# Kernel tuning notes

Hardware: AMD Instinct MI355X
Metric: run time of the kernel (lower is better)

Reference implementation:

```python
import jax, jax.numpy as jnp
import numpy as np

K = 2.0          # arctan surrogate sharpness (init kwarg k)
THRESHOLD = 1.0  # init kwarg threshold


def _binop(ei, ej):
    # linear recurrence combine: (A, Bu) pairs, v_t = A_t*v_{t-1} + Bu_t
    a_i, b_i = ei
    a_j, b_j = ej
    return a_j * a_i, a_j * b_i + b_j


def _pscan(tau, x):
    # x: [B, T, H]; tau: [H] broadcast over batch and time (matches
    # jnp.repeat(tau[None], T, 0) inside vmap over batch in the original).
    tau_b = jnp.broadcast_to(tau, x.shape)
    _, v = jax.lax.associative_scan(_binop, (tau_b, x), axis=1)
    return v


@jax.custom_vjp
def _spike(x):
    # spyx arctan surrogate: forward is Heaviside, backward 1/(1+(k*x)^2)
    return jnp.where(x > 0, 1.0, 0.0).astype(x.dtype)


def _spike_fwd(x):
    return _spike(x), x


def _spike_bwd(x, g):
    return (g / (1.0 + (K * x) ** 2),)


_spike.defvjp(_spike_fwd, _spike_bwd)


def setup_inputs() -> dict:
    key = jax.random.key(0)
    k1, k2 = jax.random.split(key)
    x = jax.random.normal(k1, (16, 1024, 1024), dtype=jnp.float32)
    # beta ~ TruncatedNormal(mean=0.25, std=0.5), as in hk.initializers
    beta = 0.25 + 0.5 * jax.random.truncated_normal(k2, -2.0, 2.0, (1024,), jnp.float32)
    return {"x": x, "beta": beta}


def reference(x, beta):
    b = jnp.clip(beta, 0.0, 1.0)
    V = _pscan(b, x)                      # membrane potential scan
    R = _pscan(b, jax.nn.sigmoid(V))      # refractory/reset scan
    return _spike(V - R - THRESHOLD), V
```

## Files before the change

kernel.cpp:

```cpp
#include <hip/hip_runtime.h>


#define BB 16
#define TT 1024
#define HH 1024
#define UNR 32

__global__ __launch_bounds__(64) void lif_scan(const float* __restrict__ x,
                                               const float* __restrict__ beta,
                                               float* __restrict__ out_spike,
                                               float* __restrict__ out_v) {
    const int tid = blockIdx.x * blockDim.x + threadIdx.x;
    const int b = tid >> 10;
    const int h = tid & (HH - 1);

    const float bf = fminf(fmaxf(beta[h], 0.0f), 1.0f);
    const double bd = (double)bf;

    const size_t base = (size_t)b * TT * HH + (size_t)h;
    const float* __restrict__ xp = x + base;
    float* __restrict__ sp = out_spike + base;
    float* __restrict__ vp = out_v + base;

    double V = 0.0, R = 0.0;

    float xbuf[UNR];
#pragma unroll
    for (int i = 0; i < UNR; ++i) xbuf[i] = xp[(size_t)i * HH];

#pragma unroll 1
    for (int t0 = 0; t0 < TT; t0 += UNR) {
        float xnext[UNR];
        const bool more = (t0 + UNR) < TT;
        if (more) {
#pragma unroll
            for (int i = 0; i < UNR; ++i)
                xnext[i] = xp[(size_t)(t0 + UNR + i) * HH];
        }
#pragma unroll
        for (int i = 0; i < UNR; ++i) {
            V = fma(bd, V, (double)xbuf[i]);
            const float vf = (float)V;
            const float s = 1.0f / (1.0f + __expf(-vf));
            R = fma(bd, R, (double)s);
            const double d = V - R;
            const size_t off = (size_t)(t0 + i) * HH;
            sp[off] = (d > 1.0) ? 1.0f : 0.0f;
            vp[off] = vf;
        }
        if (more) {
#pragma unroll
            for (int i = 0; i < UNR; ++i) xbuf[i] = xnext[i];
        }
    }
}

extern "C" void kernel_launch(void* const* d_in, const int* in_sizes, int n_in,
                              void* d_out, int out_size, void* d_ws, size_t ws_size,
                              hipStream_t stream) {
    const float* x = (const float*)d_in[0];
    const float* beta = (const float*)d_in[1];
    float* out = (float*)d_out;
    float* out_spike = out;
    float* out_v = out + (size_t)BB * TT * HH;

    const int total_threads = BB * HH;
    const int block = 64;
    const int grid = total_threads / block;
    lif_scan<<<grid, block, 0, stream>>>(x, beta, out_spike, out_v);
}
```

Measured before the change: 209.4 us.

## Split time axis into chunks with two-level chunked scan via shared memory

```diff
diff --git a/kernel.cpp b/kernel.cpp
--- a/kernel.cpp
+++ b/kernel.cpp
@@ -4,54 +4,73 @@
 #define BB 16
 #define TT 1024
 #define HH 1024
-#define UNR 32
+#define L 64
+#define C 16
+#define SEQ 64
 
-__global__ __launch_bounds__(64) void lif_scan(const float* __restrict__ x,
-                                               const float* __restrict__ beta,
-                                               float* __restrict__ out_spike,
-                                               float* __restrict__ out_v) {
-    const int tid = blockIdx.x * blockDim.x + threadIdx.x;
-    const int b = tid >> 10;
-    const int h = tid & (HH - 1);
+__global__ __launch_bounds__(1024, 4) void lif_scan(const float* __restrict__ x,
+                                                    const float* __restrict__ beta,
+                                                    float* __restrict__ out_spike,
+                                                    float* __restrict__ out_v) {
+    __shared__ double lds_sum[C][SEQ];
+
+    const int tid = threadIdx.x;
+    const int c = tid >> 6;
+    const int s = tid & 63;
+    const int blk = blockIdx.x;
+    const int b = blk >> 4;
+    const int h = ((blk & 15) << 6) + s;
 
     const float bf = fminf(fmaxf(beta[h], 0.0f), 1.0f);
     const double bd = (double)bf;
+    double pwL = bd;
+#pragma unroll
+    for (int k = 0; k < 6; ++k) pwL *= pwL;
 
-    const size_t base = (size_t)b * TT * HH + (size_t)h;
+    const size_t base = (size_t)b * TT * HH + (size_t)(c * L) * HH + (size_t)h;
     const float* __restrict__ xp = x + base;
+    float* __restrict__ vp = out_v + base;
     float* __restrict__ sp = out_spike + base;
-    float* __restrict__ vp = out_v + base;
 
-    double V = 0.0, R = 0.0;
+    float arr[L];
+#pragma unroll
+    for (int i = 0; i < L; ++i) arr[i] = xp[(size_t)i * HH];
 
-    float xbuf[UNR];
+    double Vd = 0.0;
 #pragma unroll
-    for (int i = 0; i < UNR; ++i) xbuf[i] = xp[(size_t)i * HH];
+    for (int i = 0; i < L; ++i) {
+        Vd = fma(bd, Vd, (double)arr[i]);
+        arr[i] = (float)Vd;
+    }
+    lds_sum[c][s] = Vd;
+    __syncthreads();
 
-#pragma unroll 1
-    for (int t0 = 0; t0 < TT; t0 += UNR) {
-        float xnext[UNR];
-        const bool more = (t0 + UNR) < TT;
-        if (more) {
+    double Vstart = 0.0;
+    for (int j = 0; j < c; ++j) Vstart = fma(pwL, Vstart, lds_sum[j][s]);
+    __syncthreads();
+
+    double vcarry = Vstart;
+    double Rd = 0.0;
 #pragma unroll
-            for (int i = 0; i < UNR; ++i)
-                xnext[i] = xp[(size_t)(t0 + UNR + i) * HH];
-        }
+    for (int i = 0; i < L; ++i) {
+        vcarry *= bd;
+        const float vfull = arr[i] + (float)vcarry;
+        vp[(size_t)i * HH] = vfull;
+        const float sg = 1.0f / (1.0f + __expf(-vfull));
+        Rd = fma(bd, Rd, (double)sg);
+        arr[i] = vfull - (float)Rd;
+    }
+    lds_sum[c][s] = Rd;
+    __syncthreads();
+
+    double Rstart = 0.0;
+    for (int j = 0; j < c; ++j) Rstart = fma(pwL, Rstart, lds_sum[j][s]);
+
+    double rcarry = Rstart;
 #pragma unroll
-        for (int i = 0; i < UNR; ++i) {
-            V = fma(bd, V, (double)xbuf[i]);
-            const float vf = (float)V;
-            const float s = 1.0f / (1.0f + __expf(-vf));
-            R = fma(bd, R, (double)s);
-            const double d = V - R;
-            const size_t off = (size_t)(t0 + i) * HH;
-            sp[off] = (d > 1.0) ? 1.0f : 0.0f;
-            vp[off] = vf;
-        }
-        if (more) {
-#pragma unroll
-            for (int i = 0; i < UNR; ++i) xbuf[i] = xnext[i];
-        }
+    for (int i = 0; i < L; ++i) {
+        rcarry *= bd;
+        sp[(size_t)i * HH] = (arr[i] - (float)rcarry > 1.0f) ? 1.0f : 0.0f;
     }
 }
 
@@ -64,8 +83,6 @@
     float* out_spike = out;
     float* out_v = out + (size_t)BB * TT * HH;
 
-    const int total_threads = BB * HH;
-    const int block = 64;
-    const int grid = total_threads / block;
-    lif_scan<<<grid, block, 0, stream>>>(x, beta, out_spike, out_v);
+    const int grid = (BB * HH) / SEQ;
+    lif_scan<<<grid, 1024, 0, stream>>>(x, beta, out_spike, out_v);
 }
```

After: 240.9 us. 15.1% more time.
